# Kernel tuning notes

Measured on AMD Instinct MI355X. Metric: run time of the kernel, lower is better.

Reference implementation:

```python
import jax, jax.numpy as jnp
import numpy as np

D_MODEL = 1024
N_HEADS = 16
HEAD_DIM = D_MODEL // N_HEADS
L = 2048


def setup_inputs() -> dict:
    key = jax.random.key(0)
    ks = jax.random.split(key, 7)
    x = jax.random.normal(ks[0], (L, D_MODEL), dtype=jnp.float32)
    pair_bias = jax.random.normal(ks[1], (N_HEADS, L, L), dtype=jnp.float32)
    gate = jax.random.uniform(ks[2], (N_HEADS, 1, 1), dtype=jnp.float32)
    # Learned params (Linear stores weight [out, in]; y = x @ W.T + b)
    s_qkv = 1.0 / np.sqrt(D_MODEL)
    W_qkv = jax.random.uniform(ks[3], (3 * D_MODEL, D_MODEL), minval=-s_qkv, maxval=s_qkv, dtype=jnp.float32)
    b_qkv = jax.random.uniform(ks[4], (3 * D_MODEL,), minval=-s_qkv, maxval=s_qkv, dtype=jnp.float32)
    W_out = jax.random.uniform(ks[5], (D_MODEL, D_MODEL), minval=-s_qkv, maxval=s_qkv, dtype=jnp.float32)
    b_out = jax.random.uniform(ks[6], (D_MODEL,), minval=-s_qkv, maxval=s_qkv, dtype=jnp.float32)
    return {"x": x, "pair_bias": pair_bias, "gate": gate,
            "W_qkv": W_qkv, "b_qkv": b_qkv, "W_out": W_out, "b_out": b_out}


def reference(x, pair_bias, gate, W_qkv, b_qkv, W_out, b_out):
    Lx = x.shape[0]
    scale = HEAD_DIM ** -0.5
    qkv = (x @ W_qkv.T + b_qkv).reshape(Lx, 3, N_HEADS, HEAD_DIM)
    q, k, v = qkv[:, 0], qkv[:, 1], qkv[:, 2]  # [L, H, Dh]
    logits = jnp.einsum('ihd,jhd->hij', q, k) * scale + gate * pair_bias
    attn = jax.nn.softmax(logits, axis=-1)  # dropout p=0 (eval) -> identity
    out = jnp.einsum('hij,jhd->ihd', attn, v).reshape(Lx, D_MODEL)
    return out @ W_out.T + b_out
```

## Files before the change

kernel.cpp:

```cpp
#include <hip/hip_runtime.h>
#include <cstdint>
#include <cstddef>

#define L_SEQ  2048
#define DMODEL 1024
#define NHEADS 16
#define HDIM   64
#define NQKV   3072

typedef float f32x4 __attribute__((ext_vector_type(4)));
typedef short s16x8 __attribute__((ext_vector_type(8)));

static __device__ __forceinline__ unsigned short f2bf(float f) {
  unsigned u = __float_as_uint(f);
  return (unsigned short)((u + 0x7fffu + ((u >> 16) & 1u)) >> 16);
}

static __device__ __forceinline__ void gld_lds16(void* lds, const void* g) {
  __builtin_amdgcn_global_load_lds(
      (const __attribute__((address_space(1))) void*)g,
      (__attribute__((address_space(3))) void*)lds, 16, 0, 0);
}

__global__ __launch_bounds__(256) void cvt_kernel(
    const float* __restrict__ x, const float* __restrict__ wqkv,
    const float* __restrict__ wout,
    unsigned short* __restrict__ xb, unsigned short* __restrict__ wqkvb,
    unsigned short* __restrict__ woutb) {
  const int NX = L_SEQ * DMODEL / 4;
  const int NW1 = NQKV * DMODEL / 4;
  const int NW2 = DMODEL * DMODEL / 4;
  const int tot = NX + NW1 + NW2;
  for (int i = blockIdx.x * blockDim.x + threadIdx.x; i < tot;
       i += gridDim.x * blockDim.x) {
    const float4* s;
    unsigned short* d;
    int j;
    if (i < NX) { s = (const float4*)x; d = xb; j = i; }
    else if (i < NX + NW1) { s = (const float4*)wqkv; d = wqkvb; j = i - NX; }
    else { s = (const float4*)wout; d = woutb; j = i - NX - NW1; }
    float4 v = s[j];
    ushort4 o;
    o.x = f2bf(v.x); o.y = f2bf(v.y); o.z = f2bf(v.z); o.w = f2bf(v.w);
    *(ushort4*)(d + 4 * (size_t)j) = o;
  }
}

template <int KDIM>
static __device__ __forceinline__ void gemm_bt_core(
    const unsigned short* __restrict__ A, const unsigned short* __restrict__ Bt,
    unsigned short* As, unsigned short* Bs, int bm, int bn, f32x4 acc[4][4]) {
  const int tid = threadIdx.x;
  const int lane = tid & 63;
  const int wave = tid >> 6;
  const int g = lane >> 4;
  const int li = lane & 15;
  const int wm = (wave >> 1) * 64;
  const int wn = (wave & 1) * 64;
  const int arow = tid >> 2;
  const int acolb = (tid & 3) << 4;
  const char* gA = (const char*)A + (size_t)(bm * 128 + arow) * (KDIM * 2) + acolb;
  const char* gB = (const char*)Bt + (size_t)(bn * 128 + arow) * (KDIM * 2) + acolb;
  char* lA = (char*)As + wave * 1024;
  char* lB = (char*)Bs + wave * 1024;
  const size_t half = (size_t)64 * KDIM * 2;
  for (int kt = 0; kt < KDIM; kt += 32) {
    __syncthreads();
    gld_lds16(lA, gA + kt * 2);
    gld_lds16(lA + 4096, gA + half + kt * 2);
    gld_lds16(lB, gB + kt * 2);
    gld_lds16(lB + 4096, gB + half + kt * 2);
    __syncthreads();
    const s16x8* Av = (const s16x8*)As;
    const s16x8* Bv = (const s16x8*)Bs;
    s16x8 af[4], bfv[4];
#pragma unroll
    for (int mt = 0; mt < 4; ++mt) af[mt] = Av[(wm + mt * 16 + li) * 4 + g];
#pragma unroll
    for (int nt = 0; nt < 4; ++nt) bfv[nt] = Bv[(wn + nt * 16 + li) * 4 + g];
#pragma unroll
    for (int mt = 0; mt < 4; ++mt)
#pragma unroll
      for (int nt = 0; nt < 4; ++nt)
        acc[mt][nt] = __builtin_amdgcn_mfma_f32_16x16x32_bf16(
            af[mt], bfv[nt], acc[mt][nt], 0, 0, 0);
  }
}

__global__ __launch_bounds__(256, 2) void gemm_qkv_k(
    const unsigned short* __restrict__ A, const unsigned short* __restrict__ Bt,
    const float* __restrict__ bqkv, unsigned short* __restrict__ Qb,
    unsigned short* __restrict__ Kb, unsigned short* __restrict__ Vt) {
  __shared__ alignas(16) unsigned short As[128 * 32], Bs[128 * 32];
  f32x4 acc[4][4] = {};
  gemm_bt_core<DMODEL>(A, Bt, As, Bs, blockIdx.x, blockIdx.y, acc);
  const int lane = threadIdx.x & 63, wave = threadIdx.x >> 6;
  const int g = lane >> 4, li = lane & 15;
  const int wm = (wave >> 1) * 64, wn = (wave & 1) * 64;
#pragma unroll
  for (int mt = 0; mt < 4; ++mt)
#pragma unroll
    for (int nt = 0; nt < 4; ++nt)
#pragma unroll
      for (int r = 0; r < 4; ++r) {
        int i = blockIdx.x * 128 + wm + mt * 16 + 4 * g + r;
        int n = blockIdx.y * 128 + wn + nt * 16 + li;
        float v = acc[mt][nt][r] + bqkv[n];
        int s = n >> 10;
        int h = (n >> 6) & 15;
        int d = n & 63;
        if (s == 0)      Qb[(((size_t)h * L_SEQ + i) << 6) + d] = f2bf(v * 0.125f);
        else if (s == 1) Kb[(((size_t)h * L_SEQ + i) << 6) + d] = f2bf(v);
        else             Vt[(size_t)(h * 64 + d) * L_SEQ + i] = f2bf(v);
      }
}

__global__ __launch_bounds__(256, 2) void attn_k(
    const unsigned short* __restrict__ Qb, const unsigned short* __restrict__ Kb,
    const unsigned short* __restrict__ Vt, const float* __restrict__ bias,
    const float* __restrict__ gate, unsigned short* __restrict__ AO) {
  __shared__ alignas(16) char lds[16 * 1024 + 256];
  const int h = blockIdx.y;
  const int tid = threadIdx.x, lane = tid & 63, wave = tid >> 6;
  const int g = lane >> 4, li = lane & 15;
  const int i0 = blockIdx.x * 16;
  char* myP = lds + wave * 2048;
  const s16x8* Qv = (const s16x8*)(Qb + (((size_t)h * L_SEQ + i0) << 6));
  const s16x8 qf0 = Qv[li * 8 + g];
  const s16x8 qf1 = Qv[li * 8 + 4 + g];
  const float gh = gate[h];
  const float* bh = bias + (size_t)h * L_SEQ * L_SEQ + (size_t)i0 * L_SEQ;
  const s16x8* Kall = (const s16x8*)(Kb + (((size_t)h * L_SEQ) << 6));
  f32x4 accO[4] = {};
  f32x4 lpart = {0.f, 0.f, 0.f, 0.f};

  s16x8 kf[2][8];
  float bb[2][16];

  {
    const int j0 = wave * 64;
#pragma unroll
    for (int nt = 0; nt < 4; ++nt) {
      kf[0][2 * nt] = Kall[(j0 + nt * 16 + li) * 8 + g];
      kf[0][2 * nt + 1] = Kall[(j0 + nt * 16 + li) * 8 + 4 + g];
    }
#pragma unroll
    for (int r = 0; r < 4; ++r)
#pragma unroll
      for (int nt = 0; nt < 4; ++nt)
        bb[0][4 * r + nt] = bh[(size_t)(4 * g + r) * L_SEQ + j0 + nt * 16 + li];
  }

#pragma unroll
  for (int t = 0; t < 8; ++t) {
    const int cb = t & 1, nb = cb ^ 1;
    const int j0 = t * 256 + wave * 64;
    s16x8 v0[4], v1[4];
#pragma unroll
    for (int dt = 0; dt < 4; ++dt) {
      const unsigned short* vb = Vt + (size_t)(h * 64 + dt * 16 + li) * L_SEQ + j0;
      v0[dt] = *(const s16x8*)(vb + 8 * g);
      v1[dt] = *(const s16x8*)(vb + 32 + 8 * g);
    }
    if (t < 7) {
      const int jn = j0 + 256;
#pragma unroll
      for (int r = 0; r < 4; ++r)
#pragma unroll
        for (int nt = 0; nt < 4; ++nt)
          bb[nb][4 * r + nt] =
              bh[(size_t)(4 * g + r) * L_SEQ + jn + nt * 16 + li];
    }
    f32x4 s[4];
#pragma unroll
    for (int nt = 0; nt < 4; ++nt) {
      f32x4 z = {0.f, 0.f, 0.f, 0.f};
      z = __builtin_amdgcn_mfma_f32_16x16x32_bf16(qf0, kf[cb][2 * nt], z, 0, 0, 0);
      z = __builtin_amdgcn_mfma_f32_16x16x32_bf16(qf1, kf[cb][2 * nt + 1], z, 0, 0, 0);
      s[nt] = z;
    }
    if (t < 7) {
      const int jn = j0 + 256;
#pragma unroll
      for (int nt = 0; nt < 4; ++nt) {
        kf[nb][2 * nt] = Kall[(jn + nt * 16 + li) * 8 + g];
        kf[nb][2 * nt + 1] = Kall[(jn + nt * 16 + li) * 8 + 4 + g];
      }
    }
#pragma unroll
    for (int nt = 0; nt < 4; ++nt)
#pragma unroll
      for (int r = 0; r < 4; ++r) {
        float p = __expf(fmaf(gh, bb[cb][4 * r + nt], s[nt][r]));
        lpart[r] += p;
        int row = 4 * g + r, col = nt * 16 + li;
        unsigned b = (unsigned)(row * 128 + col * 2) ^ (unsigned)((row & 7) << 4);
        *(unsigned short*)(myP + b) = f2bf(p);
      }
    asm volatile("s_waitcnt lgkmcnt(0)" ::: "memory");
    unsigned b0 = ((unsigned)(li * 128 + 16 * g)) ^ (unsigned)((li & 7) << 4);
    unsigned b1 = ((unsigned)(li * 128 + 64 + 16 * g)) ^ (unsigned)((li & 7) << 4);
    s16x8 pa0 = *(const s16x8*)(myP + b0);
    s16x8 pa1 = *(const s16x8*)(myP + b1);
#pragma unroll
    for (int dt = 0; dt < 4; ++dt) {
      accO[dt] = __builtin_amdgcn_mfma_f32_16x16x32_bf16(pa0, v0[dt], accO[dt], 0, 0, 0);
      accO[dt] = __builtin_amdgcn_mfma_f32_16x16x32_bf16(pa1, v1[dt], accO[dt], 0, 0, 0);
    }
  }
  float lrow[4];
#pragma unroll
  for (int r = 0; r < 4; ++r) {
    float tl = lpart[r];
    tl += __shfl_xor(tl, 1);
    tl += __shfl_xor(tl, 2);
    tl += __shfl_xor(tl, 4);
    tl += __shfl_xor(tl, 8);
    lrow[r] = tl;
  }
  __syncthreads();
  float* accL = (float*)lds;
  float* lL = (float*)(lds + 16 * 1024);
#pragma unroll
  for (int dt = 0; dt < 4; ++dt)
#pragma unroll
    for (int r = 0; r < 4; ++r)
      accL[(wave * 16 + 4 * g + r) * 64 + dt * 16 + li] = accO[dt][r];
  if (li == 0) {
#pragma unroll
    for (int r = 0; r < 4; ++r) lL[wave * 16 + 4 * g + r] = lrow[r];
  }
  __syncthreads();
  {
    const int row = tid >> 4;
    const int c0 = (tid & 15) * 4;
    f32x4 sum = {0.f, 0.f, 0.f, 0.f};
    float lsum = 0.f;
#pragma unroll
    for (int w = 0; w < 4; ++w) {
      const f32x4 a = *(const f32x4*)&accL[(w * 16 + row) * 64 + c0];
      sum += a;
      lsum += lL[w * 16 + row];
    }
    const float inv = 1.0f / lsum;
    ushort4 o;
    o.x = f2bf(sum[0] * inv);
    o.y = f2bf(sum[1] * inv);
    o.z = f2bf(sum[2] * inv);
    o.w = f2bf(sum[3] * inv);
    *(ushort4*)(AO + (size_t)(i0 + row) * DMODEL + h * 64 + c0) = o;
  }
}

__global__ __launch_bounds__(256, 2) void gemm_out_k(
    const unsigned short* __restrict__ A, const unsigned short* __restrict__ Bt,
    const float* __restrict__ bout, float* __restrict__ out) {
  __shared__ alignas(16) unsigned short As[128 * 32], Bs[128 * 32];
  f32x4 acc[4][4] = {};
  gemm_bt_core<DMODEL>(A, Bt, As, Bs, blockIdx.x, blockIdx.y, acc);
  const int lane = threadIdx.x & 63, wave = threadIdx.x >> 6;
  const int g = lane >> 4, li = lane & 15;
  const int wm = (wave >> 1) * 64, wn = (wave & 1) * 64;
#pragma unroll
  for (int mt = 0; mt < 4; ++mt)
#pragma unroll
    for (int nt = 0; nt < 4; ++nt)
#pragma unroll
      for (int r = 0; r < 4; ++r) {
        int i = blockIdx.x * 128 + wm + mt * 16 + 4 * g + r;
        int n = blockIdx.y * 128 + wn + nt * 16 + li;
        out[(size_t)i * DMODEL + n] = acc[mt][nt][r] + bout[n];
      }
}

extern "C" void kernel_launch(void* const* d_in, const int* in_sizes, int n_in,
                              void* d_out, int out_size, void* d_ws,
                              size_t ws_size, hipStream_t stream) {
  const float* x = (const float*)d_in[0];
  const float* pb = (const float*)d_in[1];
  const float* gate = (const float*)d_in[2];
  const float* wqkv = (const float*)d_in[3];
  const float* bqkv = (const float*)d_in[4];
  const float* wout = (const float*)d_in[5];
  const float* bout = (const float*)d_in[6];

  unsigned short* ws = (unsigned short*)d_ws;
  unsigned short* xb = ws;
  unsigned short* wqkvb = xb + (size_t)L_SEQ * DMODEL;
  unsigned short* woutb = wqkvb + (size_t)NQKV * DMODEL;
  unsigned short* Qb = woutb + (size_t)DMODEL * DMODEL;
  unsigned short* Kb = Qb + (size_t)NHEADS * L_SEQ * HDIM;
  unsigned short* Vt = Kb + (size_t)NHEADS * L_SEQ * HDIM;
  unsigned short* AO = Vt + (size_t)NHEADS * L_SEQ * HDIM;

  cvt_kernel<<<1024, 256, 0, stream>>>(x, wqkv, wout, xb, wqkvb, woutb);
  gemm_qkv_k<<<dim3(16, 24), 256, 0, stream>>>(xb, wqkvb, bqkv, Qb, Kb, Vt);
  attn_k<<<dim3(128, 16), 256, 0, stream>>>(Qb, Kb, Vt, pb, gate, AO);
  gemm_out_k<<<dim3(16, 8), 256, 0, stream>>>(AO, woutb, bout, (float*)d_out);
}
```

Baseline: 191.0 us.

## Stream pair-bias tiles into LDS via async global_load_lds triple buffer

Replaces per-thread register prefetch of the pair-bias tile with a three-stage LDS ring filled by direct global-to-LDS 16-byte loads issued two iterations ahead. Manual vmcnt waits and block barriers synchronise each stage. The goal is deeper memory latency hiding and coalesced bias reads, which dominate traffic for this bandwidth-bound attention. In exchange, LDS use grows to about 56KB per block, which may limit occupancy, and two barriers are added per iteration. The vmcnt counts must also match the number of in-flight loads exactly.

```diff
diff --git a/kernel.cpp b/kernel.cpp
--- a/kernel.cpp
+++ b/kernel.cpp
@@ -20,6 +20,13 @@
   __builtin_amdgcn_global_load_lds(
       (const __attribute__((address_space(1))) void*)g,
       (__attribute__((address_space(3))) void*)lds, 16, 0, 0);
+}
+
+template <int N>
+static __device__ __forceinline__ void wait_vm() {
+  if constexpr (N >= 8)      asm volatile("s_waitcnt vmcnt(8)" ::: "memory");
+  else if constexpr (N == 4) asm volatile("s_waitcnt vmcnt(4)" ::: "memory");
+  else                       asm volatile("s_waitcnt vmcnt(0)" ::: "memory");
 }
 
 __global__ __launch_bounds__(256) void cvt_kernel(
@@ -119,12 +126,12 @@
     const unsigned short* __restrict__ Qb, const unsigned short* __restrict__ Kb,
     const unsigned short* __restrict__ Vt, const float* __restrict__ bias,
     const float* __restrict__ gate, unsigned short* __restrict__ AO) {
-  __shared__ alignas(16) char lds[16 * 1024 + 256];
+  __shared__ alignas(16) char lds[3 * 16384 + 4 * 2048];
   const int h = blockIdx.y;
   const int tid = threadIdx.x, lane = tid & 63, wave = tid >> 6;
   const int g = lane >> 4, li = lane & 15;
   const int i0 = blockIdx.x * 16;
-  char* myP = lds + wave * 2048;
+  char* myP = lds + 3 * 16384 + wave * 2048;
   const s16x8* Qv = (const s16x8*)(Qb + (((size_t)h * L_SEQ + i0) << 6));
   const s16x8 qf0 = Qv[li * 8 + g];
   const s16x8 qf1 = Qv[li * 8 + 4 + g];
@@ -134,9 +141,18 @@
   f32x4 accO[4] = {};
   f32x4 lpart = {0.f, 0.f, 0.f, 0.f};
 
+  auto stage = [&](int t) {
+#pragma unroll
+    for (int q = 0; q < 4; ++q) {
+      const int row = 4 * wave + q;
+      gld_lds16(lds + (t % 3) * 16384 + row * 1024,
+                (const char*)(bh + (size_t)row * L_SEQ + t * 256) + lane * 16);
+    }
+  };
+
   s16x8 kf[2][8];
-  float bb[2][16];
-
+  stage(0);
+  stage(1);
   {
     const int j0 = wave * 64;
 #pragma unroll
@@ -144,32 +160,19 @@
       kf[0][2 * nt] = Kall[(j0 + nt * 16 + li) * 8 + g];
       kf[0][2 * nt + 1] = Kall[(j0 + nt * 16 + li) * 8 + 4 + g];
     }
-#pragma unroll
-    for (int r = 0; r < 4; ++r)
-#pragma unroll
-      for (int nt = 0; nt < 4; ++nt)
-        bb[0][4 * r + nt] = bh[(size_t)(4 * g + r) * L_SEQ + j0 + nt * 16 + li];
   }
 
 #pragma unroll
   for (int t = 0; t < 8; ++t) {
     const int cb = t & 1, nb = cb ^ 1;
     const int j0 = t * 256 + wave * 64;
+    if (t + 2 < 8) stage(t + 2);
     s16x8 v0[4], v1[4];
 #pragma unroll
     for (int dt = 0; dt < 4; ++dt) {
       const unsigned short* vb = Vt + (size_t)(h * 64 + dt * 16 + li) * L_SEQ + j0;
       v0[dt] = *(const s16x8*)(vb + 8 * g);
       v1[dt] = *(const s16x8*)(vb + 32 + 8 * g);
-    }
-    if (t < 7) {
-      const int jn = j0 + 256;
-#pragma unroll
-      for (int r = 0; r < 4; ++r)
-#pragma unroll
-        for (int nt = 0; nt < 4; ++nt)
-          bb[nb][4 * r + nt] =
-              bh[(size_t)(4 * g + r) * L_SEQ + jn + nt * 16 + li];
     }
     f32x4 s[4];
 #pragma unroll
@@ -187,13 +190,18 @@
         kf[nb][2 * nt + 1] = Kall[(jn + nt * 16 + li) * 8 + 4 + g];
       }
     }
+    if (t <= 5)      wait_vm<8>();
+    else if (t == 6) wait_vm<4>();
+    else             wait_vm<0>();
+    __builtin_amdgcn_s_barrier();
+    const float* bl = (const float*)(lds + (t % 3) * 16384);
 #pragma unroll
     for (int nt = 0; nt < 4; ++nt)
 #pragma unroll
       for (int r = 0; r < 4; ++r) {
-        float p = __expf(fmaf(gh, bb[cb][4 * r + nt], s[nt][r]));
+        const int row = 4 * g + r, col = nt * 16 + li;
+        float p = __expf(fmaf(gh, bl[row * 256 + wave * 64 + col], s[nt][r]));
         lpart[r] += p;
-        int row = 4 * g + r, col = nt * 16 + li;
         unsigned b = (unsigned)(row * 128 + col * 2) ^ (unsigned)((row & 7) << 4);
         *(unsigned short*)(myP + b) = f2bf(p);
       }
@@ -207,6 +215,7 @@
       accO[dt] = __builtin_amdgcn_mfma_f32_16x16x32_bf16(pa0, v0[dt], accO[dt], 0, 0, 0);
       accO[dt] = __builtin_amdgcn_mfma_f32_16x16x32_bf16(pa1, v1[dt], accO[dt], 0, 0, 0);
     }
+    __builtin_amdgcn_s_barrier();
   }
   float lrow[4];
 #pragma unroll
```

After: 206.5 us. 8.1% more time.

## Stage pair-bias through swizzled double-buffered LDS with coalesced row loads

Applied to the files above, without the earlier changes.

Each wave now loads four full bias rows with 16-byte coalesced loads and writes them into a swizzled, double-buffered LDS tile. Waves then read their columns from that tile instead of issuing scattered scalar global loads per fragment, and a block barrier is added each iteration. K fragments are no longer prefetched a tile ahead. The grid becomes 1D with a remapping that interleaves heads across blocks, and the occupancy hint rises to 3 blocks. The goal is better bandwidth on the dominant bias stream, at the cost of more LDS use and per-iteration synchronisation.

```diff
diff --git a/kernel.cpp b/kernel.cpp
--- a/kernel.cpp
+++ b/kernel.cpp
@@ -115,16 +115,19 @@
       }
 }
 
-__global__ __launch_bounds__(256, 2) void attn_k(
+__global__ __launch_bounds__(256, 3) void attn_k(
     const unsigned short* __restrict__ Qb, const unsigned short* __restrict__ Kb,
     const unsigned short* __restrict__ Vt, const float* __restrict__ bias,
     const float* __restrict__ gate, unsigned short* __restrict__ AO) {
-  __shared__ alignas(16) char lds[16 * 1024 + 256];
-  const int h = blockIdx.y;
+  __shared__ alignas(16) float blds[2][16 * 256];
+  __shared__ alignas(16) char plds[4 * 2048];
+  const int bid = blockIdx.x;
+  const int slot = bid >> 3;
+  const int h = (bid & 7) + 8 * (slot >> 7);
+  const int i0 = (slot & 127) * 16;
   const int tid = threadIdx.x, lane = tid & 63, wave = tid >> 6;
   const int g = lane >> 4, li = lane & 15;
-  const int i0 = blockIdx.x * 16;
-  char* myP = lds + wave * 2048;
+  char* myP = plds + wave * 2048;
   const s16x8* Qv = (const s16x8*)(Qb + (((size_t)h * L_SEQ + i0) << 6));
   const s16x8 qf0 = Qv[li * 8 + g];
   const s16x8 qf1 = Qv[li * 8 + 4 + g];
@@ -133,28 +136,32 @@
   const s16x8* Kall = (const s16x8*)(Kb + (((size_t)h * L_SEQ) << 6));
   f32x4 accO[4] = {};
   f32x4 lpart = {0.f, 0.f, 0.f, 0.f};
-
-  s16x8 kf[2][8];
-  float bb[2][16];
+  const int swzg = (g << 2) | ((g & 1) << 4);
+  const int srow = 4 * wave;
 
   {
-    const int j0 = wave * 64;
+    f32x4 rb[4];
+#pragma unroll
+    for (int q = 0; q < 4; ++q)
+      rb[q] = *(const f32x4*)(bh + (size_t)(srow + q) * L_SEQ + 4 * lane);
+#pragma unroll
+    for (int q = 0; q < 4; ++q) {
+      const int rr = srow + q, G = (rr >> 2) & 3;
+      const int sw = (G << 2) | ((G & 1) << 4);
+      *(f32x4*)&blds[0][rr * 256 + ((4 * lane) ^ sw)] = rb[q];
+    }
+    asm volatile("s_waitcnt lgkmcnt(0)" ::: "memory");
+  }
+
+#pragma unroll
+  for (int t = 0; t < 8; ++t) {
+    const int j0 = t * 256 + wave * 64;
+    s16x8 k0[4], k1[4];
 #pragma unroll
     for (int nt = 0; nt < 4; ++nt) {
-      kf[0][2 * nt] = Kall[(j0 + nt * 16 + li) * 8 + g];
-      kf[0][2 * nt + 1] = Kall[(j0 + nt * 16 + li) * 8 + 4 + g];
-    }
-#pragma unroll
-    for (int r = 0; r < 4; ++r)
-#pragma unroll
-      for (int nt = 0; nt < 4; ++nt)
-        bb[0][4 * r + nt] = bh[(size_t)(4 * g + r) * L_SEQ + j0 + nt * 16 + li];
-  }
-
-#pragma unroll
-  for (int t = 0; t < 8; ++t) {
-    const int cb = t & 1, nb = cb ^ 1;
-    const int j0 = t * 256 + wave * 64;
+      k0[nt] = Kall[(j0 + nt * 16 + li) * 8 + g];
+      k1[nt] = Kall[(j0 + nt * 16 + li) * 8 + 4 + g];
+    }
     s16x8 v0[4], v1[4];
 #pragma unroll
     for (int dt = 0; dt < 4; ++dt) {
@@ -162,51 +169,54 @@
       v0[dt] = *(const s16x8*)(vb + 8 * g);
       v1[dt] = *(const s16x8*)(vb + 32 + 8 * g);
     }
+    f32x4 rb[4];
     if (t < 7) {
-      const int jn = j0 + 256;
-#pragma unroll
-      for (int r = 0; r < 4; ++r)
-#pragma unroll
-        for (int nt = 0; nt < 4; ++nt)
-          bb[nb][4 * r + nt] =
-              bh[(size_t)(4 * g + r) * L_SEQ + jn + nt * 16 + li];
-    }
+#pragma unroll
+      for (int q = 0; q < 4; ++q)
+        rb[q] = *(const f32x4*)(bh + (size_t)(srow + q) * L_SEQ +
+                                (t + 1) * 256 + 4 * lane);
+    }
+    __builtin_amdgcn_s_barrier();
     f32x4 s[4];
 #pragma unroll
     for (int nt = 0; nt < 4; ++nt) {
       f32x4 z = {0.f, 0.f, 0.f, 0.f};
-      z = __builtin_amdgcn_mfma_f32_16x16x32_bf16(qf0, kf[cb][2 * nt], z, 0, 0, 0);
-      z = __builtin_amdgcn_mfma_f32_16x16x32_bf16(qf1, kf[cb][2 * nt + 1], z, 0, 0, 0);
+      z = __builtin_amdgcn_mfma_f32_16x16x32_bf16(qf0, k0[nt], z, 0, 0, 0);
+      z = __builtin_amdgcn_mfma_f32_16x16x32_bf16(qf1, k1[nt], z, 0, 0, 0);
       s[nt] = z;
     }
-    if (t < 7) {
-      const int jn = j0 + 256;
-#pragma unroll
-      for (int nt = 0; nt < 4; ++nt) {
-        kf[nb][2 * nt] = Kall[(jn + nt * 16 + li) * 8 + g];
-        kf[nb][2 * nt + 1] = Kall[(jn + nt * 16 + li) * 8 + 4 + g];
-      }
-    }
+    const float* bl = blds[t & 1];
 #pragma unroll
     for (int nt = 0; nt < 4; ++nt)
 #pragma unroll
       for (int r = 0; r < 4; ++r) {
-        float p = __expf(fmaf(gh, bb[cb][4 * r + nt], s[nt][r]));
+        const int row = 4 * g + r;
+        const int cc = wave * 64 + nt * 16 + li;
+        float p = __expf(fmaf(gh, bl[row * 256 + (cc ^ swzg)], s[nt][r]));
         lpart[r] += p;
-        int row = 4 * g + r, col = nt * 16 + li;
-        unsigned b = (unsigned)(row * 128 + col * 2) ^ (unsigned)((row & 7) << 4);
+        unsigned b = (unsigned)(row * 128 + (nt * 16 + li) * 2) ^
+                     (unsigned)((row & 7) << 4);
         *(unsigned short*)(myP + b) = f2bf(p);
       }
     asm volatile("s_waitcnt lgkmcnt(0)" ::: "memory");
-    unsigned b0 = ((unsigned)(li * 128 + 16 * g)) ^ (unsigned)((li & 7) << 4);
-    unsigned b1 = ((unsigned)(li * 128 + 64 + 16 * g)) ^ (unsigned)((li & 7) << 4);
-    s16x8 pa0 = *(const s16x8*)(myP + b0);
-    s16x8 pa1 = *(const s16x8*)(myP + b1);
+    const unsigned b0 = ((unsigned)(li * 128 + 16 * g)) ^ (unsigned)((li & 7) << 4);
+    const unsigned b1 = ((unsigned)(li * 128 + 64 + 16 * g)) ^ (unsigned)((li & 7) << 4);
+    const s16x8 pa0 = *(const s16x8*)(myP + b0);
+    const s16x8 pa1 = *(const s16x8*)(myP + b1);
 #pragma unroll
     for (int dt = 0; dt < 4; ++dt) {
       accO[dt] = __builtin_amdgcn_mfma_f32_16x16x32_bf16(pa0, v0[dt], accO[dt], 0, 0, 0);
       accO[dt] = __builtin_amdgcn_mfma_f32_16x16x32_bf16(pa1, v1[dt], accO[dt], 0, 0, 0);
     }
+    if (t < 7) {
+#pragma unroll
+      for (int q = 0; q < 4; ++q) {
+        const int rr = srow + q, G = (rr >> 2) & 3;
+        const int sw = (G << 2) | ((G & 1) << 4);
+        *(f32x4*)&blds[(t + 1) & 1][rr * 256 + ((4 * lane) ^ sw)] = rb[q];
+      }
+    }
+    asm volatile("s_waitcnt lgkmcnt(0)" ::: "memory");
   }
   float lrow[4];
 #pragma unroll
@@ -219,8 +229,8 @@
     lrow[r] = tl;
   }
   __syncthreads();
-  float* accL = (float*)lds;
-  float* lL = (float*)(lds + 16 * 1024);
+  float* accL = &blds[0][0];
+  float* lL = &blds[1][0];
 #pragma unroll
   for (int dt = 0; dt < 4; ++dt)
 #pragma unroll
@@ -295,6 +305,6 @@
 
   cvt_kernel<<<1024, 256, 0, stream>>>(x, wqkv, wout, xb, wqkvb, woutb);
   gemm_qkv_k<<<dim3(16, 24), 256, 0, stream>>>(xb, wqkvb, bqkv, Qb, Kb, Vt);
-  attn_k<<<dim3(128, 16), 256, 0, stream>>>(Qb, Kb, Vt, pb, gate, AO);
+  attn_k<<<2048, 256, 0, stream>>>(Qb, Kb, Vt, pb, gate, AO);
   gemm_out_k<<<dim3(16, 8), 256, 0, stream>>>(AO, woutb, bout, (float*)d_out);
 }
```

Result: slower. 333.5 us (+74.6%).
